# Optimization experiments

Hardware: AMD Instinct MI355X
Metric: run time of the kernel (lower is better)

The kernel has to match this reference:

```python
import jax, jax.numpy as jnp
import numpy as np

N, G, S = 51200, 128, 400  # nodes, graphs, nodes-per-graph
E, IN, H, OUT = 819200, 128, 128, 10


def _graph_conv(x, src, dst, W_rel, b_rel, W_root):
    # PyG GraphConv (aggr='add'): lin_rel(sum_{j->i} x_j) + lin_root(x_i)
    agg = jax.ops.segment_sum(x[src], dst, num_segments=N)  # [N, d]
    return agg @ W_rel + b_rel + x @ W_root


def _mixup(x, lam, perm):
    return x * lam + (1.0 - lam) * x[perm]


def setup_inputs() -> dict:
    key = jax.random.key(0)
    ks = jax.random.split(key, 12)
    rng = np.random.default_rng(0)

    x0 = jax.random.normal(ks[0], (N, IN), dtype=jnp.float32)
    edge_index = jax.random.randint(ks[1], (2, E), 0, N, dtype=jnp.int64)
    lam = jax.random.uniform(ks[2], (1,), dtype=jnp.float32)
    ptr = jnp.arange(0, N + 1, S, dtype=jnp.int64)            # [G+1]
    batch = jnp.repeat(jnp.arange(G, dtype=jnp.int64), S)     # [N]

    def seg_perm():
        return jnp.asarray(np.concatenate(
            [g * S + rng.permutation(S) for g in range(G)]), dtype=jnp.int64)

    perm1, perm2, perm3 = seg_perm(), seg_perm(), seg_perm()

    def lin(k, fan_in, fan_out):
        bound = 1.0 / np.sqrt(fan_in)
        return jax.random.uniform(k, (fan_in, fan_out), jnp.float32, -bound, bound)

    params = {
        'W1_rel': lin(ks[3], IN, H), 'b1_rel': jnp.zeros((H,), jnp.float32),
        'W1_root': lin(ks[4], IN, H),
        'W2_rel': lin(ks[5], H, H), 'b2_rel': jnp.zeros((H,), jnp.float32),
        'W2_root': lin(ks[6], H, H),
        'W_lin': lin(ks[7], H, OUT), 'b_lin': jnp.zeros((OUT,), jnp.float32),
    }
    return dict(x0=x0, edge_index=edge_index, lam=lam, ptr=ptr, batch=batch,
                perm1=perm1, perm2=perm2, perm3=perm3, **params)


def reference(x0, edge_index, lam, ptr, batch, perm1, perm2, perm3,
              W1_rel, b1_rel, W1_root, W2_rel, b2_rel, W2_root, W_lin, b_lin):
    src, dst = edge_index[0], edge_index[1]
    l = lam[0]

    x1 = jax.nn.relu(_graph_conv(x0, src, dst, W1_rel, b1_rel, W1_root))
    x1 = _mixup(x1, l, perm1)  # dropout p=0.4 is identity in eval mode

    x2 = jax.nn.relu(_graph_conv(x1, src, dst, W2_rel, b2_rel, W2_root))
    x2 = _mixup(x2, l, perm2)

    # NOTE: original forward reuses conv2 for the third layer (conv3 unused)
    x3 = jax.nn.relu(_graph_conv(x2, src, dst, W2_rel, b2_rel, W2_root))
    x3 = _mixup(x3, l, perm3)

    pooled = jax.ops.segment_sum(x3, batch, num_segments=G)  # [G, H]
    logits = pooled @ W_lin + b_lin                          # [G, OUT]
    return jax.nn.log_softmax(logits, axis=-1)
```

## Files before the change

kernel.cpp:

```cpp
#include <hip/hip_runtime.h>

#define N_NODES 51200
#define N_EDGES 819200
#define HDIM 128
#define AK 256
#define NGRAPH 128
#define SEG 400
#define NOUT 10
#define SLOT 64

typedef unsigned short ushort_t;
typedef unsigned int uint_t;
typedef __attribute__((ext_vector_type(8))) short bf16x8;
typedef __attribute__((ext_vector_type(16))) float f32x16;

static __device__ __forceinline__ unsigned short f2bf(float f) {
    unsigned int u = __float_as_uint(f);
    unsigned int r = (u + 0x7fffu + ((u >> 16) & 1u)) >> 16;
    return (unsigned short)r;
}
static __device__ __forceinline__ float bf2f(unsigned short h) {
    return __uint_as_float(((unsigned int)h) << 16);
}


__global__ void k_prep(const float* __restrict__ x, ushort_t* __restrict__ Abuf,
                       const float* __restrict__ W1rel, const float* __restrict__ W1root,
                       const float* __restrict__ W2rel, const float* __restrict__ W2root,
                       ushort_t* __restrict__ Wfrag1, ushort_t* __restrict__ Wfrag2,
                       float* __restrict__ pooled, int* __restrict__ cnt) {
    int b = blockIdx.x;
    if (b < 6400) {
        int idx = b * 256 + threadIdx.x;
        int row = idx >> 5;
        int c4 = (idx & 31) * 4;
        float4 v = *(const float4*)(x + (size_t)row * HDIM + c4);
        ushort4 h;
        h.x = f2bf(v.x); h.y = f2bf(v.y); h.z = f2bf(v.z); h.w = f2bf(v.w);
        *(ushort4*)(Abuf + (size_t)row * AK + HDIM + c4) = h;
    } else if (b < 6656) {
        int w2 = (b >= 6528);
        int tid = (b - (w2 ? 6528 : 6400)) * 256 + threadIdx.x;
        const float* Wrel  = w2 ? W2rel : W1rel;
        const float* Wroot = w2 ? W2root : W1root;
        ushort_t* dstF     = w2 ? Wfrag2 : Wfrag1;
        int j = tid & 7;
        int l = (tid >> 3) & 63;
        int s = (tid >> 9) & 15;
        int t = tid >> 13;
        int k = 16 * s + (l >> 5) * 8 + j;
        int n = 32 * t + (l & 31);
        float v = (k < HDIM) ? Wrel[(size_t)k * HDIM + n]
                             : Wroot[(size_t)(k - HDIM) * HDIM + n];
        dstF[tid] = f2bf(v);
    } else if (b < 6720) {
        int i = (b - 6656) * 256 + threadIdx.x;
        pooled[i] = 0.f;
    } else {
        int i = (b - 6720) * 256 + threadIdx.x;
        cnt[i] = 0;
    }
}


__global__ void k_scatter(const int* __restrict__ src, const int* __restrict__ dst,
                          int* __restrict__ cnt, ushort_t* __restrict__ col2) {
    int base = blockIdx.x * 1024 + threadIdx.x;
    int d[4], p[4];
#pragma unroll
    for (int k = 0; k < 4; ++k) d[k] = dst[base + k * 256];
#pragma unroll
    for (int k = 0; k < 4; ++k) p[k] = atomicAdd(&cnt[d[k]], 1);
#pragma unroll
    for (int k = 0; k < 4; ++k)
        col2[(size_t)d[k] * SLOT + p[k]] = (ushort_t)src[base + k * 256];
}


__global__ __launch_bounds__(256) void k_aggregate(ushort_t* __restrict__ Abuf,
                                                   const int* __restrict__ cnt,
                                                   const ushort_t* __restrict__ col) {
    int wave = threadIdx.x >> 6;
    int lane = threadIdx.x & 63;
    int il = lane & 15;
    int qe = lane >> 4;
    int node = blockIdx.x * 4 + wave;
    int beg = node * SLOT;
    int end = beg + cnt[node];

    const ushort_t* xsrc = Abuf + HDIM + (size_t)il * 8;

    float a[4][8];
#pragma unroll
    for (int j = 0; j < 4; ++j)
#pragma unroll
        for (int k = 0; k < 8; ++k) a[j][k] = 0.f;

    int e = beg;
    for (; e + 16 <= end; e += 16) {
        int c[4];
#pragma unroll
        for (int j = 0; j < 4; ++j) c[j] = (int)col[e + 4 * j + qe];
#pragma unroll
        for (int j = 0; j < 4; ++j) {
            uint4 v = *(const uint4*)(xsrc + (size_t)c[j] * AK);
            a[j][0] += __uint_as_float(v.x << 16);
            a[j][1] += __uint_as_float(v.x & 0xffff0000u);
            a[j][2] += __uint_as_float(v.y << 16);
            a[j][3] += __uint_as_float(v.y & 0xffff0000u);
            a[j][4] += __uint_as_float(v.z << 16);
            a[j][5] += __uint_as_float(v.z & 0xffff0000u);
            a[j][6] += __uint_as_float(v.w << 16);
            a[j][7] += __uint_as_float(v.w & 0xffff0000u);
        }
    }
    for (; e + 4 <= end; e += 4) {
        int c = (int)col[e + qe];
        uint4 v = *(const uint4*)(xsrc + (size_t)c * AK);
        a[0][0] += __uint_as_float(v.x << 16);
        a[0][1] += __uint_as_float(v.x & 0xffff0000u);
        a[0][2] += __uint_as_float(v.y << 16);
        a[0][3] += __uint_as_float(v.y & 0xffff0000u);
        a[0][4] += __uint_as_float(v.z << 16);
        a[0][5] += __uint_as_float(v.z & 0xffff0000u);
        a[0][6] += __uint_as_float(v.w << 16);
        a[0][7] += __uint_as_float(v.w & 0xffff0000u);
    }
    if (e < end) {
        int idx = e + qe;
        bool ok = idx < end;
        int c = (int)col[ok ? idx : e];
        uint4 v = *(const uint4*)(xsrc + (size_t)c * AK);
        a[1][0] += ok ? __uint_as_float(v.x << 16) : 0.f;
        a[1][1] += ok ? __uint_as_float(v.x & 0xffff0000u) : 0.f;
        a[1][2] += ok ? __uint_as_float(v.y << 16) : 0.f;
        a[1][3] += ok ? __uint_as_float(v.y & 0xffff0000u) : 0.f;
        a[1][4] += ok ? __uint_as_float(v.z << 16) : 0.f;
        a[1][5] += ok ? __uint_as_float(v.z & 0xffff0000u) : 0.f;
        a[1][6] += ok ? __uint_as_float(v.w << 16) : 0.f;
        a[1][7] += ok ? __uint_as_float(v.w & 0xffff0000u) : 0.f;
    }

    float s[8];
#pragma unroll
    for (int k = 0; k < 8; ++k) {
        s[k] = (a[0][k] + a[1][k]) + (a[2][k] + a[3][k]);
        s[k] += __shfl_xor(s[k], 16);
        s[k] += __shfl_xor(s[k], 32);
    }

    if (qe == 0) {
        uint4 o;
        o.x = (uint_t)f2bf(s[0]) | ((uint_t)f2bf(s[1]) << 16);
        o.y = (uint_t)f2bf(s[2]) | ((uint_t)f2bf(s[3]) << 16);
        o.z = (uint_t)f2bf(s[4]) | ((uint_t)f2bf(s[5]) << 16);
        o.w = (uint_t)f2bf(s[6]) | ((uint_t)f2bf(s[7]) << 16);
        *(uint4*)(Abuf + (size_t)node * AK + il * 8) = o;
    }
}


__global__ __launch_bounds__(64) void k_gemm_mfma(const ushort_t* __restrict__ Abuf,
                                                  const ushort_t* __restrict__ Wfrag,
                                                  const float* __restrict__ bias,
                                                  ushort_t* __restrict__ y) {
    __shared__ ushort_t sm[32][72];
    int lane = threadIdx.x;
    int nh = blockIdx.x & 1;
    int row0 = (blockIdx.x >> 1) * 32;
    int m = lane & 31;
    int half = lane >> 5;

    f32x16 acc[2];
#pragma unroll
    for (int t = 0; t < 2; ++t) acc[t] = (f32x16)(0.f);

    float bb[2];
#pragma unroll
    for (int t = 0; t < 2; ++t) bb[t] = bias[nh * 64 + t * 32 + m];

    const ushort_t* arow = Abuf + (size_t)(row0 + m) * AK + half * 8;
    const ushort_t* wf = Wfrag + (size_t)lane * 8 + (size_t)nh * 2 * 16 * 512;

#pragma unroll
    for (int s = 0; s < 16; ++s) {
        bf16x8 afrag = *(const bf16x8*)(arow + s * 16);
#pragma unroll
        for (int t = 0; t < 2; ++t) {
            bf16x8 bfrag = *(const bf16x8*)(wf + (size_t)(t * 16 + s) * 512);
            acc[t] = __builtin_amdgcn_mfma_f32_32x32x16_bf16(afrag, bfrag, acc[t], 0, 0, 0);
        }
    }

#pragma unroll
    for (int t = 0; t < 2; ++t) {
#pragma unroll
        for (int r = 0; r < 16; ++r) {
            int rowL = (r & 3) + 8 * (r >> 2) + 4 * half;
            sm[rowL][t * 32 + m] = f2bf(fmaxf(acc[t][r] + bb[t], 0.f));
        }
    }
    __syncthreads();
    int seg = lane & 7;
    int rbase = lane >> 3;
#pragma unroll
    for (int it = 0; it < 4; ++it) {
        int rowL = rbase + it * 8;
        int4 chunk = *(const int4*)&sm[rowL][seg * 8];
        *(int4*)(y + (size_t)(row0 + rowL) * HDIM + nh * 64 + seg * 8) = chunk;
    }
}


__global__ __launch_bounds__(64) void k_gemm_pool(const ushort_t* __restrict__ Abuf,
                                                  const ushort_t* __restrict__ Wfrag,
                                                  const float* __restrict__ bias,
                                                  float* __restrict__ pooled) {
    int lane = threadIdx.x;
    int nh = blockIdx.x & 1;
    int row0 = (blockIdx.x >> 1) * 32;
    int m = lane & 31;
    int half = lane >> 5;

    f32x16 acc[2];
#pragma unroll
    for (int t = 0; t < 2; ++t) acc[t] = (f32x16)(0.f);

    float bb[2];
#pragma unroll
    for (int t = 0; t < 2; ++t) bb[t] = bias[nh * 64 + t * 32 + m];

    const ushort_t* arow = Abuf + (size_t)(row0 + m) * AK + half * 8;
    const ushort_t* wf = Wfrag + (size_t)lane * 8 + (size_t)nh * 2 * 16 * 512;

#pragma unroll
    for (int s = 0; s < 16; ++s) {
        bf16x8 afrag = *(const bf16x8*)(arow + s * 16);
#pragma unroll
        for (int t = 0; t < 2; ++t) {
            bf16x8 bfrag = *(const bf16x8*)(wf + (size_t)(t * 16 + s) * 512);
            acc[t] = __builtin_amdgcn_mfma_f32_32x32x16_bf16(afrag, bfrag, acc[t], 0, 0, 0);
        }
    }

    int g0 = row0 / SEG;
    int bnd = (g0 + 1) * SEG;
    int straddle = (row0 + 31 >= bnd);

#pragma unroll
    for (int t = 0; t < 2; ++t) {
        float s0 = 0.f, s1 = 0.f;
#pragma unroll
        for (int r = 0; r < 16; ++r) {
            int row = row0 + (r & 3) + 8 * (r >> 2) + 4 * half;
            float v = fmaxf(acc[t][r] + bb[t], 0.f);
            if (row < bnd) s0 += v; else s1 += v;
        }
        s0 += __shfl_xor(s0, 32);
        s1 += __shfl_xor(s1, 32);
        if (half == 0) {
            int coln = nh * 64 + t * 32 + m;
            atomicAdd(&pooled[g0 * HDIM + coln], s0);
            if (straddle) atomicAdd(&pooled[(g0 + 1) * HDIM + coln], s1);
        }
    }
}


__global__ void k_mixup_toA(const ushort_t* __restrict__ y, const int* __restrict__ perm,
                            const float* __restrict__ lam, ushort_t* __restrict__ Abuf) {
    int idx = blockIdx.x * 256 + threadIdx.x;
    int row = idx >> 5;
    int c4 = (idx & 31) * 4;
    float l = lam[0];
    float om = 1.f - l;
    int p = perm[row];
    ushort4 a = *(const ushort4*)(y + (size_t)row * HDIM + c4);
    ushort4 b = *(const ushort4*)(y + (size_t)p * HDIM + c4);
    ushort4 o;
    o.x = f2bf(l * bf2f(a.x) + om * bf2f(b.x));
    o.y = f2bf(l * bf2f(a.y) + om * bf2f(b.y));
    o.z = f2bf(l * bf2f(a.z) + om * bf2f(b.z));
    o.w = f2bf(l * bf2f(a.w) + om * bf2f(b.w));
    *(ushort4*)(Abuf + (size_t)row * AK + HDIM + c4) = o;
}


__global__ __launch_bounds__(64) void k_final(const float* __restrict__ pooled,
                                              const float* __restrict__ Wlin,
                                              const float* __restrict__ blin,
                                              float* __restrict__ out) {
    int g = blockIdx.x;
    int lane = threadIdx.x;
    float2 v = *(const float2*)(pooled + (size_t)g * HDIM + lane * 2);
    float p[NOUT];
#pragma unroll
    for (int o = 0; o < NOUT; ++o)
        p[o] = v.x * Wlin[(size_t)(2 * lane) * NOUT + o] +
               v.y * Wlin[(size_t)(2 * lane + 1) * NOUT + o];
#pragma unroll
    for (int mask = 1; mask < 64; mask <<= 1)
#pragma unroll
        for (int o = 0; o < NOUT; ++o) p[o] += __shfl_xor(p[o], mask);
    if (lane == 0) {
        float lg[NOUT];
        float mx = -1e30f;
#pragma unroll
        for (int o = 0; o < NOUT; ++o) { lg[o] = p[o] + blin[o]; mx = fmaxf(mx, lg[o]); }
        float se = 0.f;
#pragma unroll
        for (int o = 0; o < NOUT; ++o) se += expf(lg[o] - mx);
        float lse = mx + logf(se);
#pragma unroll
        for (int o = 0; o < NOUT; ++o) out[g * NOUT + o] = lg[o] - lse;
    }
}


extern "C" void kernel_launch(void* const* d_in, const int* in_sizes, int n_in,
                              void* d_out, int out_size, void* d_ws, size_t ws_size,
                              hipStream_t stream) {
    const float* x0     = (const float*)d_in[0];
    const int*   edge   = (const int*)d_in[1];
    const int*   src    = edge;
    const int*   dst    = edge + N_EDGES;
    const float* lam    = (const float*)d_in[2];
    const int*   perm1  = (const int*)d_in[5];
    const int*   perm2  = (const int*)d_in[6];
    const float* W1_rel = (const float*)d_in[8];
    const float* b1_rel = (const float*)d_in[9];
    const float* W1_root= (const float*)d_in[10];
    const float* W2_rel = (const float*)d_in[11];
    const float* b2_rel = (const float*)d_in[12];
    const float* W2_root= (const float*)d_in[13];
    const float* W_lin  = (const float*)d_in[14];
    const float* b_lin  = (const float*)d_in[15];
    float* out = (float*)d_out;

    char* w = (char*)d_ws;
    size_t off = 0;
    auto alloc = [&](size_t bytes) -> void* {
        void* p = w + off;
        off = (off + bytes + 255) & ~(size_t)255;
        return p;
    };
    int* cnt       = (int*)alloc((size_t)N_NODES * 4);
    ushort_t* col2 = (ushort_t*)alloc((size_t)N_NODES * SLOT * 2);
    ushort_t* Abuf   = (ushort_t*)alloc((size_t)N_NODES * AK * 2);
    ushort_t* ybuf   = (ushort_t*)alloc((size_t)N_NODES * HDIM * 2);
    ushort_t* Wfrag1 = (ushort_t*)alloc(32768 * 2);
    ushort_t* Wfrag2 = (ushort_t*)alloc(32768 * 2);
    float* pooled    = (float*)alloc((size_t)NGRAPH * HDIM * 4);

    k_prep<<<6920, 256, 0, stream>>>(x0, Abuf, W1_rel, W1_root, W2_rel, W2_root,
                                     Wfrag1, Wfrag2, pooled, cnt);
    k_scatter<<<N_EDGES / 1024, 256, 0, stream>>>(src, dst, cnt, col2);

    const int aggGrid  = N_NODES / 4;
    const int gemmGrid = (N_NODES / 32) * 2;
    const int elGrid   = (N_NODES * HDIM / 4) / 256;

    k_aggregate<<<aggGrid, 256, 0, stream>>>(Abuf, cnt, col2);
    k_gemm_mfma<<<gemmGrid, 64, 0, stream>>>(Abuf, Wfrag1, b1_rel, ybuf);
    k_mixup_toA<<<elGrid, 256, 0, stream>>>(ybuf, perm1, lam, Abuf);
    k_aggregate<<<aggGrid, 256, 0, stream>>>(Abuf, cnt, col2);
    k_gemm_mfma<<<gemmGrid, 64, 0, stream>>>(Abuf, Wfrag2, b2_rel, ybuf);
    k_mixup_toA<<<elGrid, 256, 0, stream>>>(ybuf, perm2, lam, Abuf);
    k_aggregate<<<aggGrid, 256, 0, stream>>>(Abuf, cnt, col2);
    k_gemm_pool<<<gemmGrid, 64, 0, stream>>>(Abuf, Wfrag2, b2_rel, pooled);

    k_final<<<NGRAPH, 64, 0, stream>>>(pooled, W_lin, b_lin, out);
}
```

Measured before the change: 299.6 us.

## Replace global-atomic edge scatter with LDS histogram count, prefix and place

Replaces the single scatter kernel, which did one global atomicAdd per edge on the per-node counter, with a three-pass counting sort. Per-block shared-memory histograms use 8-bit packed counters, a prefix kernel turns them into per-block offsets and final degrees, and a place kernel fills col2 using LDS atomics. This is meant to cut contention on global atomics at the cost of two extra launches and a histogram buffer that reuses ybuf. It assumes per-node degree stays below 256, so each packed byte cannot overflow.

```diff
diff --git a/kernel.cpp b/kernel.cpp
--- a/kernel.cpp
+++ b/kernel.cpp
@@ -9,6 +9,12 @@
 #define NOUT 10
 #define SLOT 64
 
+#define HISTW (N_NODES / 4)
+#define NBLK 200
+#define EPB (N_EDGES / NBLK)
+#define SEGS 8
+#define BPSEG (NBLK / SEGS)
+
 typedef unsigned short ushort_t;
 typedef unsigned int uint_t;
 typedef __attribute__((ext_vector_type(8))) short bf16x8;
@@ -28,7 +34,7 @@
                        const float* __restrict__ W1rel, const float* __restrict__ W1root,
                        const float* __restrict__ W2rel, const float* __restrict__ W2root,
                        ushort_t* __restrict__ Wfrag1, ushort_t* __restrict__ Wfrag2,
-                       float* __restrict__ pooled, int* __restrict__ cnt) {
+                       float* __restrict__ pooled) {
     int b = blockIdx.x;
     if (b < 6400) {
         int idx = b * 256 + threadIdx.x;
@@ -53,27 +59,93 @@
         float v = (k < HDIM) ? Wrel[(size_t)k * HDIM + n]
                              : Wroot[(size_t)(k - HDIM) * HDIM + n];
         dstF[tid] = f2bf(v);
-    } else if (b < 6720) {
+    } else {
         int i = (b - 6656) * 256 + threadIdx.x;
         pooled[i] = 0.f;
-    } else {
-        int i = (b - 6720) * 256 + threadIdx.x;
-        cnt[i] = 0;
-    }
-}
-
-
-__global__ void k_scatter(const int* __restrict__ src, const int* __restrict__ dst,
-                          int* __restrict__ cnt, ushort_t* __restrict__ col2) {
-    int base = blockIdx.x * 1024 + threadIdx.x;
-    int d[4], p[4];
-#pragma unroll
-    for (int k = 0; k < 4; ++k) d[k] = dst[base + k * 256];
-#pragma unroll
-    for (int k = 0; k < 4; ++k) p[k] = atomicAdd(&cnt[d[k]], 1);
-#pragma unroll
-    for (int k = 0; k < 4; ++k)
-        col2[(size_t)d[k] * SLOT + p[k]] = (ushort_t)src[base + k * 256];
+    }
+}
+
+
+__global__ __launch_bounds__(256) void k_count(const int* __restrict__ dst,
+                                               uint_t* __restrict__ bh) {
+    __shared__ uint_t hist[HISTW];
+    int b = blockIdx.x, tid = threadIdx.x;
+    for (int i = tid; i < HISTW; i += 256) hist[i] = 0u;
+    __syncthreads();
+    const int4* d4 = (const int4*)dst + b * (EPB / 4);
+#pragma unroll
+    for (int p = 0; p < 4; ++p) {
+        int4 d = d4[p * 256 + tid];
+        atomicAdd(&hist[((uint_t)d.x) >> 2], 1u << ((d.x & 3) * 8));
+        atomicAdd(&hist[((uint_t)d.y) >> 2], 1u << ((d.y & 3) * 8));
+        atomicAdd(&hist[((uint_t)d.z) >> 2], 1u << ((d.z & 3) * 8));
+        atomicAdd(&hist[((uint_t)d.w) >> 2], 1u << ((d.w & 3) * 8));
+    }
+    __syncthreads();
+    for (int i = tid; i < HISTW; i += 256) bh[(size_t)b * HISTW + i] = hist[i];
+}
+
+
+__global__ __launch_bounds__(256) void k_prefix(uint_t* __restrict__ bh,
+                                                int* __restrict__ cnt) {
+    __shared__ uint_t segsum[SEGS][32];
+    int ci = threadIdx.x & 31;
+    int seg = threadIdx.x >> 5;
+    int c = blockIdx.x * 32 + ci;
+    uint_t v[BPSEG];
+    uint_t sum = 0;
+#pragma unroll
+    for (int k = 0; k < BPSEG; ++k) {
+        v[k] = bh[(size_t)(seg * BPSEG + k) * HISTW + c];
+        sum += v[k];
+    }
+    segsum[seg][ci] = sum;
+    __syncthreads();
+    uint_t run = 0;
+    for (int s = 0; s < seg; ++s) run += segsum[s][ci];
+#pragma unroll
+    for (int k = 0; k < BPSEG; ++k) {
+        bh[(size_t)(seg * BPSEG + k) * HISTW + c] = run;
+        run += v[k];
+    }
+    if (seg == SEGS - 1) {
+        int4 o;
+        o.x = (int)(run & 0xffu);
+        o.y = (int)((run >> 8) & 0xffu);
+        o.z = (int)((run >> 16) & 0xffu);
+        o.w = (int)((run >> 24) & 0xffu);
+        *(int4*)(cnt + 4 * c) = o;
+    }
+}
+
+
+__global__ __launch_bounds__(256) void k_place(const int* __restrict__ src,
+                                               const int* __restrict__ dst,
+                                               const uint_t* __restrict__ bh,
+                                               ushort_t* __restrict__ col2) {
+    __shared__ uint_t hist[HISTW];
+    int b = blockIdx.x, tid = threadIdx.x;
+    for (int i = tid; i < HISTW; i += 256) hist[i] = bh[(size_t)b * HISTW + i];
+    __syncthreads();
+    const int4* d4 = (const int4*)dst + b * (EPB / 4);
+    const int4* s4 = (const int4*)src + b * (EPB / 4);
+#pragma unroll
+    for (int p = 0; p < 4; ++p) {
+        int4 d = d4[p * 256 + tid];
+        int4 s = s4[p * 256 + tid];
+#define PLACE1(dd, ss)                                                        \
+        do {                                                                  \
+            uint_t w = (uint_t)(dd);                                          \
+            int sh = (int)(w & 3u) * 8;                                       \
+            uint_t old = atomicAdd(&hist[w >> 2], 1u << sh);                  \
+            col2[(size_t)w * SLOT + ((old >> sh) & 0xffu)] = (ushort_t)(ss);  \
+        } while (0)
+        PLACE1(d.x, s.x);
+        PLACE1(d.y, s.y);
+        PLACE1(d.z, s.z);
+        PLACE1(d.w, s.w);
+#undef PLACE1
+    }
 }
 
 
@@ -352,9 +424,13 @@
     ushort_t* Wfrag2 = (ushort_t*)alloc(32768 * 2);
     float* pooled    = (float*)alloc((size_t)NGRAPH * HDIM * 4);
 
-    k_prep<<<6920, 256, 0, stream>>>(x0, Abuf, W1_rel, W1_root, W2_rel, W2_root,
-                                     Wfrag1, Wfrag2, pooled, cnt);
-    k_scatter<<<N_EDGES / 1024, 256, 0, stream>>>(src, dst, cnt, col2);
+    uint_t* bh = (uint_t*)ybuf;
+
+    k_prep<<<6720, 256, 0, stream>>>(x0, Abuf, W1_rel, W1_root, W2_rel, W2_root,
+                                     Wfrag1, Wfrag2, pooled);
+    k_count<<<NBLK, 256, 0, stream>>>(dst, bh);
+    k_prefix<<<HISTW / 32, 256, 0, stream>>>(bh, cnt);
+    k_place<<<NBLK, 256, 0, stream>>>(src, dst, bh, col2);
 
     const int aggGrid  = N_NODES / 4;
     const int gemmGrid = (N_NODES / 32) * 2;
```

New measurement: 279.7 us. 1.07x faster.
